# Performance work log

Hardware: AMD Instinct MI355X
Metric: run time of the kernel (lower is better)

The kernel has to match this reference:

```python
import jax, jax.numpy as jnp
import numpy as np
import math

D_MODEL = 512
D_STATE = 64
CHUNK = 4
NC = D_MODEL // CHUNK  # 128 chunks
B_SZ, L_SEQ = 8, 4096


def setup_inputs() -> dict:
    key = jax.random.key(0)
    ks = jax.random.split(key, 10)
    x = jax.random.normal(ks[0], (B_SZ, L_SEQ, D_MODEL), dtype=jnp.float32)
    # LayerNorm params
    ln_gamma = jnp.ones((D_MODEL,), jnp.float32)
    ln_beta = jnp.zeros((D_MODEL,), jnp.float32)
    # in/out projections (stored so that y = x @ W + b)
    Win = jax.random.normal(ks[1], (D_MODEL, D_MODEL), jnp.float32) / math.sqrt(D_MODEL)
    bin_ = jnp.zeros((D_MODEL,), jnp.float32)
    Wout = jax.random.normal(ks[2], (D_MODEL, D_MODEL), jnp.float32) / math.sqrt(D_MODEL)
    bout = jnp.zeros((D_MODEL,), jnp.float32)
    # S4 core params, batched over NC chunks (faithful to S4Core init)
    Lambda_re = -0.5 * jnp.ones((NC, D_STATE), jnp.float32)
    Lambda_im = jnp.broadcast_to(jnp.arange(D_STATE, dtype=jnp.float32) * 2.0 * math.pi / D_STATE, (NC, D_STATE))
    Bmat = jax.random.normal(ks[3], (NC, D_STATE), jnp.float32)
    C_re = jax.random.normal(ks[4], (NC, D_STATE), jnp.float32)
    C_im = jax.random.normal(ks[5], (NC, D_STATE), jnp.float32)
    Dvec = jax.random.normal(ks[6], (NC,), jnp.float32)
    return {"x": x, "ln_gamma": ln_gamma, "ln_beta": ln_beta, "Win": Win, "bin_": bin_,
            "Wout": Wout, "bout": bout, "Lambda_re": Lambda_re, "Lambda_im": Lambda_im,
            "Bmat": Bmat, "C_re": C_re, "C_im": C_im, "Dvec": Dvec}


def _layernorm(x, g, b, eps=1e-5):
    mu = jnp.mean(x, axis=-1, keepdims=True)
    var = jnp.mean((x - mu) ** 2, axis=-1, keepdims=True)
    return (x - mu) * jax.lax.rsqrt(var + eps) * g + b


def reference(x, ln_gamma, ln_beta, Win, bin_, Wout, bout, Lambda_re, Lambda_im, Bmat, C_re, C_im, Dvec):
    Bsz, L, Dm = x.shape
    nc, n = Lambda_re.shape
    cs = Dm // nc

    z = _layernorm(x, ln_gamma, ln_beta)
    z = z @ Win + bin_  # in_projection

    # --- batched S4 kernel generation over all chunks ---
    omega = jnp.arange(L, dtype=jnp.float32)  # [L]
    Lam = Lambda_re + 1j * Lambda_im                     # [nc, n]
    expo = jnp.exp(Lam[:, :, None] * omega[None, None])  # [nc, n, L] complex
    CB = (C_re + 1j * C_im) * Bmat                        # [nc, n]
    k = jnp.real(jnp.einsum('cn,cnl->cl', CB, expo))      # [nc, L]
    # bidirectional: concat kernel with its flip (length 2L)
    k2 = jnp.concatenate([k, k[:, ::-1]], axis=1)         # [nc, 2L]

    # --- FFT convolution along sequence dim ---
    kf = jnp.fft.rfft(k2, n=2 * L, axis=1)                # [nc, L+1]
    u = z.reshape(Bsz, L, nc, cs)
    uf = jnp.fft.rfft(u, n=2 * L, axis=1)                 # [B, L+1, nc, cs]
    yf = uf * kf.T[None, :, :, None]                      # broadcast kernel per chunk
    y = jnp.fft.irfft(yf, n=2 * L, axis=1)[:, :L]         # [B, L, nc, cs]
    y = y + u * Dvec[None, None, :, None]                 # skip term D
    y = y.reshape(Bsz, L, Dm)

    y = y @ Wout + bout  # out_projection
    y = jax.nn.gelu(y, approximate=False)  # F.gelu default (erf)
    # dropout is identity in eval mode
    return x + y
```

## Files before the change

kernel.cpp:

```cpp
#include <hip/hip_runtime.h>
#include <hip/hip_bf16.h>
#include <stdint.h>


typedef __bf16 bf16x8 __attribute__((ext_vector_type(8)));
typedef float f32x4 __attribute__((ext_vector_type(4)));

__device__ __forceinline__ float bfu(unsigned short h) {
  return __uint_as_float(((unsigned int)h) << 16);
}
__device__ __forceinline__ unsigned short f2bf(float f) {
  unsigned int u = __float_as_uint(f);
  return (unsigned short)((u + 0x7fffu + ((u >> 16) & 1u)) >> 16);
}
__device__ __forceinline__ float lo16(unsigned int u) { return __uint_as_float(u << 16); }
__device__ __forceinline__ float hi16(unsigned int u) { return __uint_as_float(u & 0xffff0000u); }
__device__ __forceinline__ unsigned int pack2(float a, float b) {
  return (unsigned int)f2bf(a) | ((unsigned int)f2bf(b) << 16);
}

__global__ __launch_bounds__(1024) void transpose512(
    const float* __restrict__ Win, const float* __restrict__ Wout,
    unsigned short* __restrict__ WinT, unsigned short* __restrict__ WoutT) {
  __shared__ float tile[32][33];
  const float* src = blockIdx.z ? Wout : Win;
  unsigned short* dst = blockIdx.z ? WoutT : WinT;
  int x = blockIdx.x * 32 + threadIdx.x;
  int y = blockIdx.y * 32 + threadIdx.y;
  tile[threadIdx.y][threadIdx.x] = src[y * 512 + x];
  __syncthreads();
  int tx = blockIdx.y * 32 + threadIdx.x;
  int ty = blockIdx.x * 32 + threadIdx.y;
  dst[ty * 512 + tx] = f2bf(tile[threadIdx.x][threadIdx.y]);
}

__global__ __launch_bounds__(256) void kgen(
    const float* __restrict__ Lre, const float* __restrict__ Lim,
    const float* __restrict__ Bm, const float* __restrict__ Cre,
    const float* __restrict__ Cim, float* __restrict__ kk) {
  const int w = blockIdx.x * 4 + (threadIdx.x >> 6);
  const int c = w >> 5;
  const float j = (float)(w & 31);
  const int n = threadIdx.x & 63;
  const int o = c * 64 + n;
  const float cr = Cre[o] * Bm[o], ci = Cim[o] * Bm[o];
  const float e = __expf(Lre[o] * j);
  float sn, cs;
  __sincosf(Lim[o] * j, &sn, &cs);
  float t = e * (cr * cs - ci * sn);
#pragma unroll
  for (int off = 32; off > 0; off >>= 1) t += __shfl_xor(t, off);
  if (n == 0) kk[c * 32 + (w & 31)] = t;
}

__global__ __launch_bounds__(256) void ln_kernel(
    const float* __restrict__ x, unsigned short* __restrict__ z,
    const float* __restrict__ gamma, const float* __restrict__ beta) {
  const int lane = threadIdx.x & 63;
  const size_t row = (size_t)blockIdx.x * 4 + (threadIdx.x >> 6);
  const float* xr = x + row * 512 + lane * 8;
  float4 x0 = *(const float4*)xr;
  float4 x1 = *(const float4*)(xr + 4);
  float v[8] = {x0.x, x0.y, x0.z, x0.w, x1.x, x1.y, x1.z, x1.w};
  float s = 0.f, s2 = 0.f;
#pragma unroll
  for (int i = 0; i < 8; ++i) { s += v[i]; s2 += v[i] * v[i]; }
#pragma unroll
  for (int off = 32; off > 0; off >>= 1) {
    s += __shfl_xor(s, off);
    s2 += __shfl_xor(s2, off);
  }
  const float mu = s * (1.f / 512.f);
  const float var = s2 * (1.f / 512.f) - mu * mu;
  const float rstd = rsqrtf(var + 1e-5f);
  float4 g0 = *(const float4*)(gamma + lane * 8);
  float4 g1 = *(const float4*)(gamma + lane * 8 + 4);
  float4 b0 = *(const float4*)(beta + lane * 8);
  float4 b1 = *(const float4*)(beta + lane * 8 + 4);
  float g[8] = {g0.x, g0.y, g0.z, g0.w, g1.x, g1.y, g1.z, g1.w};
  float b[8] = {b0.x, b0.y, b0.z, b0.w, b1.x, b1.y, b1.z, b1.w};
  float o[8];
#pragma unroll
  for (int i = 0; i < 8; ++i) o[i] = (v[i] - mu) * rstd * g[i] + b[i];
  uint4 ov;
  ov.x = pack2(o[0], o[1]); ov.y = pack2(o[2], o[3]);
  ov.z = pack2(o[4], o[5]); ov.w = pack2(o[6], o[7]);
  *(uint4*)(z + row * 512 + lane * 8) = ov;
}

template <int EPI>
__global__ __launch_bounds__(256, 4) void gemm_bt(
    const unsigned short* __restrict__ A, const unsigned short* __restrict__ Bt,
    const float* __restrict__ bias, const float* __restrict__ X,
    unsigned short* __restrict__ Out16, float* __restrict__ OutF) {
  __shared__ alignas(16) unsigned short lA[128 * 32];
  __shared__ alignas(16) unsigned short lB[128 * 32];
  const int tid = threadIdx.x;
  const int wave = tid >> 6;
  const int lane = tid & 63;
  const int m0 = blockIdx.x * 128;
  const int n0 = blockIdx.y * 128;
  const int wm = (wave & 1) * 64;
  const int wn = (wave >> 1) * 64;
  const int srow = tid >> 2;
  const int sc = tid & 3;
  const int swz = (sc ^ ((srow >> 1) & 3)) * 8;

  const unsigned short* Ap0 = A + (size_t)(m0 + srow) * 512 + sc * 8;
  const unsigned short* Ap1 = Ap0 + (size_t)64 * 512;
  const unsigned short* Bp0 = Bt + (size_t)(n0 + srow) * 512 + sc * 8;
  const unsigned short* Bp1 = Bp0 + (size_t)64 * 512;

  f32x4 acc[4][4];
  const f32x4 vzero = {0.f, 0.f, 0.f, 0.f};
#pragma unroll
  for (int i = 0; i < 4; ++i)
#pragma unroll
    for (int j = 0; j < 4; ++j) acc[i][j] = vzero;

  int offA[4], offB[4];
#pragma unroll
  for (int i = 0; i < 4; ++i) {
    const int rA = wm + i * 16 + (lane & 15);
    const int rB = wn + i * 16 + (lane & 15);
    offA[i] = rA * 32 + (((lane >> 4) ^ ((rA >> 1) & 3)) * 8);
    offB[i] = rB * 32 + (((lane >> 4) ^ ((rB >> 1) & 3)) * 8);
  }

  uint4 ra0 = *(const uint4*)Ap0;
  uint4 ra1 = *(const uint4*)Ap1;
  uint4 rb0 = *(const uint4*)Bp0;
  uint4 rb1 = *(const uint4*)Bp1;

  for (int k0 = 0; k0 < 512; k0 += 32) {
    __syncthreads();
    *(uint4*)&lA[srow * 32 + swz] = ra0;
    *(uint4*)&lA[(64 + srow) * 32 + swz] = ra1;
    *(uint4*)&lB[srow * 32 + swz] = rb0;
    *(uint4*)&lB[(64 + srow) * 32 + swz] = rb1;
    __syncthreads();
    if (k0 + 32 < 512) {
      ra0 = *(const uint4*)(Ap0 + k0 + 32);
      ra1 = *(const uint4*)(Ap1 + k0 + 32);
      rb0 = *(const uint4*)(Bp0 + k0 + 32);
      rb1 = *(const uint4*)(Bp1 + k0 + 32);
    }
    bf16x8 af[4], bfr[4];
#pragma unroll
    for (int mi = 0; mi < 4; ++mi) af[mi] = *(const bf16x8*)&lA[offA[mi]];
#pragma unroll
    for (int ni = 0; ni < 4; ++ni) bfr[ni] = *(const bf16x8*)&lB[offB[ni]];
#pragma unroll
    for (int mi = 0; mi < 4; ++mi)
#pragma unroll
      for (int ni = 0; ni < 4; ++ni)
        acc[mi][ni] = __builtin_amdgcn_mfma_f32_16x16x32_bf16(af[mi], bfr[ni],
                                                              acc[mi][ni], 0, 0, 0);
  }

  const int cq = lane >> 4;
  const int cc = lane & 15;
#pragma unroll
  for (int mi = 0; mi < 4; ++mi) {
#pragma unroll
    for (int ni = 0; ni < 4; ++ni) {
      const int col = n0 + wn + ni * 16 + cc;
      const float bvv = bias[col];
#pragma unroll
      for (int r = 0; r < 4; ++r) {
        const size_t row = (size_t)(m0 + wm + mi * 16 + cq * 4 + r);
        float v = acc[mi][ni][r] + bvv;
        if (EPI) {
          float y = 0.79788456f * (v + 0.044715f * v * v * v);
          float e2 = __expf(2.f * y);
          float th = 1.f - 2.f / (e2 + 1.f);
          float gel = 0.5f * v * (1.f + th);
          OutF[row * 512 + col] = gel + X[row * 512 + col];
        } else {
          Out16[row * 512 + col] = f2bf(v);
        }
      }
    }
  }
}

#define CT 256
#define CD 16
#define SROW 328
__global__ __launch_bounds__(256) void conv_kernel(
    const unsigned short* __restrict__ u, const float* __restrict__ kk,
    const float* __restrict__ Dvec, unsigned short* __restrict__ y) {
  __shared__ alignas(16) unsigned short su[CD * SROW];
  __shared__ float skt[4 * 36];
  const int tid = threadIdx.x;
  const int b = blockIdx.z;
  const int t0 = blockIdx.x * CT;
  const int d0 = blockIdx.y * CD;
  const int c0 = d0 >> 2;

  if (tid < 128) {
    const int c = tid >> 5, j = tid & 31;
    skt[c * 36 + j] = kk[(c0 + c) * 32 + j];
  }
  const size_t ubase = (size_t)b * 4096 * 512;
#pragma unroll
  for (int p = 0; p < 3; ++p) {
    const int r = p * 128 + (tid >> 1);
    if (p < 2 || tid < 128) {
      const int dh = (tid & 1) * 8;
      const int t = t0 - 32 + r;
      uint4 w = make_uint4(0u, 0u, 0u, 0u);
      if (t >= 0 && t < 4096)
        w = *(const uint4*)(u + ubase + (size_t)t * 512 + d0 + dh);
      const unsigned short* ws = (const unsigned short*)&w;
#pragma unroll
      for (int q = 0; q < 8; ++q) su[(dh + q) * SROW + r] = ws[q];
    }
  }
  __syncthreads();

  const int dl = tid & 15;
  const int tseg = tid >> 4;
  const int cl = dl >> 2;
  const unsigned short* swin = &su[dl * SROW + tseg * 16];
  const float* kt = &skt[cl * 36];

  float U[88], acc[16];
#pragma unroll
  for (int p = 0; p < 11; ++p) {
    uint4 w = *(const uint4*)(swin + p * 8);
    U[p * 8 + 0] = lo16(w.x); U[p * 8 + 1] = hi16(w.x);
    U[p * 8 + 2] = lo16(w.y); U[p * 8 + 3] = hi16(w.y);
    U[p * 8 + 4] = lo16(w.z); U[p * 8 + 5] = hi16(w.z);
    U[p * 8 + 6] = lo16(w.w); U[p * 8 + 7] = hi16(w.w);
  }
  const float dv = Dvec[c0 + cl];
#pragma unroll
  for (int i = 0; i < 16; ++i) acc[i] = dv * U[32 + i];
#pragma unroll
  for (int j = 0; j < 32; ++j) {
    const float kj = kt[j];
#pragma unroll
    for (int i = 0; i < 16; ++i) acc[i] += kj * U[32 + i - j];
  }
#pragma unroll
  for (int j = 0; j < 32; ++j) {
    const float kj = kt[j];
#pragma unroll
    for (int i = 0; i < 16; ++i) acc[i] += kj * U[33 + i + j];
  }
  const int ta = t0 + tseg * 16;
  unsigned short* yp = y + ubase + (size_t)ta * 512 + d0 + dl;
#pragma unroll
  for (int i = 0; i < 16; ++i) yp[(size_t)i * 512] = f2bf(acc[i]);
}

extern "C" void kernel_launch(void* const* d_in, const int* in_sizes, int n_in,
                              void* d_out, int out_size, void* d_ws, size_t ws_size,
                              hipStream_t stream) {
  const float* x    = (const float*)d_in[0];
  const float* ln_g = (const float*)d_in[1];
  const float* ln_b = (const float*)d_in[2];
  const float* Win  = (const float*)d_in[3];
  const float* bin_ = (const float*)d_in[4];
  const float* Wout = (const float*)d_in[5];
  const float* bout = (const float*)d_in[6];
  const float* Lre  = (const float*)d_in[7];
  const float* Lim  = (const float*)d_in[8];
  const float* Bm   = (const float*)d_in[9];
  const float* Cre  = (const float*)d_in[10];
  const float* Cim  = (const float*)d_in[11];
  const float* Dv   = (const float*)d_in[12];
  float* out = (float*)d_out;

  char* ws = (char*)d_ws;
  unsigned short* bufZ  = (unsigned short*)ws;
  unsigned short* bufU  = bufZ + 16777216;
  unsigned short* WinT  = bufU + 16777216;
  unsigned short* WoutT = WinT + 512 * 512;
  float* kk             = (float*)(WoutT + 512 * 512);

  transpose512<<<dim3(16, 16, 2), dim3(32, 32), 0, stream>>>(Win, Wout, WinT, WoutT);
  kgen<<<1024, 256, 0, stream>>>(Lre, Lim, Bm, Cre, Cim, kk);
  ln_kernel<<<8192, 256, 0, stream>>>(x, bufZ, ln_g, ln_b);
  gemm_bt<0><<<dim3(256, 4), 256, 0, stream>>>(bufZ, WinT, bin_, nullptr, bufU, nullptr);
  conv_kernel<<<dim3(16, 32, 8), 256, 0, stream>>>(bufU, kk, Dv, bufZ);
  gemm_bt<1><<<dim3(256, 4), 256, 0, stream>>>(bufZ, WoutT, bout, x, nullptr, out);
}
```

Before: 230.9 us.

## Load GEMM MFMA fragments directly from global memory, drop LDS staging

Removes the shared-memory tiles and barriers from the bf16 GEMM. Each wave now loads its A and B MFMA fragments straight from global memory, with the K loop fully unrolled, and the launch-bounds occupancy hint drops from 4 to 3. This removes the LDS writes and reads and the per-iteration __syncthreads. In exchange, waves that share rows fetch the same data separately and rely on L1/L2 to absorb the redundant traffic, and register pressure rises.

```diff
diff --git a/kernel.cpp b/kernel.cpp
--- a/kernel.cpp
+++ b/kernel.cpp
@@ -89,12 +89,10 @@
 }
 
 template <int EPI>
-__global__ __launch_bounds__(256, 4) void gemm_bt(
+__global__ __launch_bounds__(256, 3) void gemm_bt(
     const unsigned short* __restrict__ A, const unsigned short* __restrict__ Bt,
     const float* __restrict__ bias, const float* __restrict__ X,
     unsigned short* __restrict__ Out16, float* __restrict__ OutF) {
-  __shared__ alignas(16) unsigned short lA[128 * 32];
-  __shared__ alignas(16) unsigned short lB[128 * 32];
   const int tid = threadIdx.x;
   const int wave = tid >> 6;
   const int lane = tid & 63;
@@ -102,14 +100,16 @@
   const int n0 = blockIdx.y * 128;
   const int wm = (wave & 1) * 64;
   const int wn = (wave >> 1) * 64;
-  const int srow = tid >> 2;
-  const int sc = tid & 3;
-  const int swz = (sc ^ ((srow >> 1) & 3)) * 8;
-
-  const unsigned short* Ap0 = A + (size_t)(m0 + srow) * 512 + sc * 8;
-  const unsigned short* Ap1 = Ap0 + (size_t)64 * 512;
-  const unsigned short* Bp0 = Bt + (size_t)(n0 + srow) * 512 + sc * 8;
-  const unsigned short* Bp1 = Bp0 + (size_t)64 * 512;
+  const int mr = lane & 15;
+  const int kq = (lane >> 4) * 8;
+
+  const unsigned short* Aw[4];
+  const unsigned short* Bw[4];
+#pragma unroll
+  for (int i = 0; i < 4; ++i) {
+    Aw[i] = A + (size_t)(m0 + wm + i * 16 + mr) * 512 + kq;
+    Bw[i] = Bt + (size_t)(n0 + wn + i * 16 + mr) * 512 + kq;
+  }
 
   f32x4 acc[4][4];
   const f32x4 vzero = {0.f, 0.f, 0.f, 0.f};
@@ -118,38 +118,14 @@
 #pragma unroll
     for (int j = 0; j < 4; ++j) acc[i][j] = vzero;
 
-  int offA[4], offB[4];
-#pragma unroll
-  for (int i = 0; i < 4; ++i) {
-    const int rA = wm + i * 16 + (lane & 15);
-    const int rB = wn + i * 16 + (lane & 15);
-    offA[i] = rA * 32 + (((lane >> 4) ^ ((rA >> 1) & 3)) * 8);
-    offB[i] = rB * 32 + (((lane >> 4) ^ ((rB >> 1) & 3)) * 8);
-  }
-
-  uint4 ra0 = *(const uint4*)Ap0;
-  uint4 ra1 = *(const uint4*)Ap1;
-  uint4 rb0 = *(const uint4*)Bp0;
-  uint4 rb1 = *(const uint4*)Bp1;
-
-  for (int k0 = 0; k0 < 512; k0 += 32) {
-    __syncthreads();
-    *(uint4*)&lA[srow * 32 + swz] = ra0;
-    *(uint4*)&lA[(64 + srow) * 32 + swz] = ra1;
-    *(uint4*)&lB[srow * 32 + swz] = rb0;
-    *(uint4*)&lB[(64 + srow) * 32 + swz] = rb1;
-    __syncthreads();
-    if (k0 + 32 < 512) {
-      ra0 = *(const uint4*)(Ap0 + k0 + 32);
-      ra1 = *(const uint4*)(Ap1 + k0 + 32);
-      rb0 = *(const uint4*)(Bp0 + k0 + 32);
-      rb1 = *(const uint4*)(Bp1 + k0 + 32);
+#pragma unroll
+  for (int kk = 0; kk < 16; ++kk) {
+    bf16x8 af[4], bfr[4];
+#pragma unroll
+    for (int i = 0; i < 4; ++i) {
+      af[i] = *(const bf16x8*)(Aw[i] + kk * 32);
+      bfr[i] = *(const bf16x8*)(Bw[i] + kk * 32);
     }
-    bf16x8 af[4], bfr[4];
-#pragma unroll
-    for (int mi = 0; mi < 4; ++mi) af[mi] = *(const bf16x8*)&lA[offA[mi]];
-#pragma unroll
-    for (int ni = 0; ni < 4; ++ni) bfr[ni] = *(const bf16x8*)&lB[offB[ni]];
 #pragma unroll
     for (int mi = 0; mi < 4; ++mi)
 #pragma unroll
```

New measurement: 304.4 us. 1.32x slower.
